# Optimization experiments

Hardware: AMD Instinct MI355X
Metric: run time of the kernel (lower is better)

The kernel has to match this reference:

```python
import jax, jax.numpy as jnp
import numpy as np

ATOM_DIM, HID, N_LAYERS, N_HEADS, PF_DIM = 34, 256, 2, 8, 1024
B, NA, NP = 32, 512, 1024


def setup_inputs() -> dict:
    key = jax.random.key(0)
    ks = iter(jax.random.split(key, 32))
    def rn(shape, s=0.02):
        return jax.random.normal(next(ks), shape, dtype=jnp.float32) * s
    L = N_LAYERS
    z = lambda *s: jnp.zeros(s, jnp.float32)
    return {
        "trg": jax.random.normal(next(ks), (B, NA, ATOM_DIM), dtype=jnp.float32),
        "src": jax.random.normal(next(ks), (B, NP, HID), dtype=jnp.float32),
        "ft_w": rn((HID, ATOM_DIM)), "ft_b": z(HID),
        "ln_g": jnp.ones((L, HID), jnp.float32), "ln_b": z(L, HID),
        "sa_wq": rn((L, HID, HID)), "sa_bq": z(L, HID),
        "sa_wk": rn((L, HID, HID)), "sa_bk": z(L, HID),
        "sa_wv": rn((L, HID, HID)), "sa_bv": z(L, HID),
        "sa_wf": rn((L, HID, HID)), "sa_bf": z(L, HID),
        "ea_wq": rn((L, HID, HID)), "ea_bq": z(L, HID),
        "ea_wk": rn((L, HID, HID)), "ea_bk": z(L, HID),
        "ea_wv": rn((L, HID, HID)), "ea_bv": z(L, HID),
        "ea_wf": rn((L, HID, HID)), "ea_bf": z(L, HID),
        "pf_w1": rn((L, PF_DIM, HID)), "pf_b1": z(L, PF_DIM),
        "pf_w2": rn((L, HID, PF_DIM)), "pf_b2": z(L, HID),
        "fc1_w": rn((256, HID)), "fc1_b": z(256),
        "fc2_w": rn((2, 256)), "fc2_b": z(2),
    }


def _ln(x, g, b, eps=1e-5):
    m = jnp.mean(x, axis=-1, keepdims=True)
    v = jnp.mean(jnp.square(x - m), axis=-1, keepdims=True)
    return (x - m) * jax.lax.rsqrt(v + eps) * g + b


def _attn(xq, xkv, wq, bq, wk, bk, wv, bv, wf, bf):
    b_, lq, h = xq.shape
    d = h // N_HEADS
    q = (xq @ wq.T + bq).reshape(b_, lq, N_HEADS, d).transpose(0, 2, 1, 3)
    k = (xkv @ wk.T + bk).reshape(b_, -1, N_HEADS, d).transpose(0, 2, 1, 3)
    v = (xkv @ wv.T + bv).reshape(b_, -1, N_HEADS, d).transpose(0, 2, 1, 3)
    scale = jnp.sqrt(jnp.float32(d))  # TransformerCPI: sqrt(hid_dim // n_heads)
    a = jax.nn.softmax(jnp.einsum('bhqd,bhkd->bhqk', q, k) / scale, axis=-1)
    o = jnp.einsum('bhqk,bhkd->bhqd', a, v).transpose(0, 2, 1, 3).reshape(b_, lq, h)
    return o @ wf.T + bf


def reference(trg, src, ft_w, ft_b, ln_g, ln_b,
              sa_wq, sa_bq, sa_wk, sa_bk, sa_wv, sa_bv, sa_wf, sa_bf,
              ea_wq, ea_bq, ea_wk, ea_bk, ea_wv, ea_bv, ea_wf, ea_bf,
              pf_w1, pf_b1, pf_w2, pf_b2, fc1_w, fc1_b, fc2_w, fc2_b):
    x = trg @ ft_w.T + ft_b  # [B, NA, HID]
    for l in range(N_LAYERS):
        x = _ln(x + _attn(x, x, sa_wq[l], sa_bq[l], sa_wk[l], sa_bk[l],
                          sa_wv[l], sa_bv[l], sa_wf[l], sa_bf[l]), ln_g[l], ln_b[l])
        x = _ln(x + _attn(x, src, ea_wq[l], ea_bq[l], ea_wk[l], ea_bk[l],
                          ea_wv[l], ea_bv[l], ea_wf[l], ea_bf[l]), ln_g[l], ln_b[l])
        h = jax.nn.relu(x @ pf_w1[l].T + pf_b1[l]) @ pf_w2[l].T + pf_b2[l]
        x = _ln(x + h, ln_g[l], ln_b[l])
    # norm-weighted attention pooling (replaces the nested Python loops)
    w = jax.nn.softmax(jnp.linalg.norm(x, axis=2), axis=1)  # [B, NA]
    pooled = jnp.einsum('bn,bnh->bh', w, x)  # [B, HID]
    return jax.nn.relu(pooled @ fc1_w.T + fc1_b) @ fc2_w.T + fc2_b
```

## Files before the change

kernel.cpp:

```cpp
#include <hip/hip_runtime.h>
#include <hip/hip_bf16.h>
#include <math.h>

#define B_   32
#define NA   512
#define NP   1024
#define HID  256
#define NH   8
#define DH   32
#define PF   1024

typedef short bf16x8 __attribute__((ext_vector_type(8)));
typedef float f32x4  __attribute__((ext_vector_type(4)));
typedef float f32x16 __attribute__((ext_vector_type(16)));

#define ZERO16 {0.f,0.f,0.f,0.f,0.f,0.f,0.f,0.f,0.f,0.f,0.f,0.f,0.f,0.f,0.f,0.f}

static __device__ inline unsigned short f2bf(float f) {
    __hip_bfloat16 h = __float2bfloat16(f);
    unsigned short u;
    __builtin_memcpy(&u, &h, 2);
    return u;
}
static __device__ inline bf16x8 pack8(float4 a, float4 b) {
    bf16x8 r;
    r[0] = (short)f2bf(a.x); r[1] = (short)f2bf(a.y);
    r[2] = (short)f2bf(a.z); r[3] = (short)f2bf(a.w);
    r[4] = (short)f2bf(b.x); r[5] = (short)f2bf(b.y);
    r[6] = (short)f2bf(b.z); r[7] = (short)f2bf(b.w);
    return r;
}

__global__ __launch_bounds__(256) void ft_kernel(const float* __restrict__ trg,
    const float* __restrict__ w, const float* __restrict__ b,
    float* __restrict__ out, unsigned short* __restrict__ outb)
{
    __shared__ float Ws[256][35];
    int tid = threadIdx.x;
    for (int k = 0; k < 34; ++k) Ws[tid][k] = w[tid*34 + k];
    float bias = b[tid];
    __syncthreads();
    int m0 = blockIdx.x * 32;
    for (int r = 0; r < 32; ++r) {
        int m = m0 + r;
        const float* tr = trg + (size_t)m*34;
        float acc = bias;
        #pragma unroll
        for (int k = 0; k < 34; ++k) acc += tr[k] * Ws[tid][k];
        out [(size_t)m*HID + tid] = acc;
        outb[(size_t)m*HID + tid] = f2bf(acc);
    }
}

__global__ __launch_bounds__(256) void cvt_bf16(const float* __restrict__ in,
    unsigned short* __restrict__ outb, int n8)
{
    int i = blockIdx.x*256 + threadIdx.x;
    int stride = gridDim.x*256;
    for (; i < n8; i += stride) {
        float4 a = *(const float4*)(in + (size_t)i*8);
        float4 b = *(const float4*)(in + (size_t)i*8 + 4);
        *(bf16x8*)(outb + (size_t)i*8) = pack8(a, b);
    }
}

__global__ __launch_bounds__(256) void cvt_w(
    const float* __restrict__ s0, const float* __restrict__ s1,
    const float* __restrict__ s2, const float* __restrict__ s3,
    const float* __restrict__ s4, const float* __restrict__ s5,
    const float* __restrict__ s6, const float* __restrict__ s7,
    const float* __restrict__ s8, const float* __restrict__ s9,
    unsigned short* __restrict__ dst)
{
    const int z = blockIdx.z;
    const float* src;
    switch (z) {
        case 0: src = s0; break; case 1: src = s1; break;
        case 2: src = s2; break; case 3: src = s3; break;
        case 4: src = s4; break; case 5: src = s5; break;
        case 6: src = s6; break; case 7: src = s7; break;
        case 8: src = s8; break; default: src = s9; break;
    }
    const int n8 = (z < 8) ? 16384 : 65536;
    const size_t off = (z < 8) ? (size_t)z*131072 : (1048576u + (size_t)(z-8)*524288);
    unsigned short* o = dst + off;
    int i = blockIdx.x*256 + threadIdx.x;
    const int stride = gridDim.x*256;
    for (; i < n8; i += stride) {
        float4 a = *(const float4*)(src + (size_t)i*8);
        float4 b = *(const float4*)(src + (size_t)i*8 + 4);
        *(bf16x8*)(o + (size_t)i*8) = pack8(a, b);
    }
}

static __device__ inline void gemm_core(const unsigned short* __restrict__ Ab,
    const unsigned short* __restrict__ Wb, const float* __restrict__ bias,
    void* __restrict__ Cv, int M, int N, int K, int mode, int L, float oscale,
    int bx, int by)
{
    __shared__ __attribute__((aligned(16))) unsigned short As[128][72];
    __shared__ __attribute__((aligned(16))) unsigned short Bs[64][72];
    const int tid = threadIdx.x;
    const int wave = tid >> 6, lane = tid & 63, lq = lane & 15, g = lane >> 4;
    const int wr = wave >> 1, wc = wave & 1;
    const int m0 = by * 128, n0 = bx * 64;

    const int ar = tid >> 1, ac = (tid & 1) * 32;
    const int br = tid >> 2, bc = (tid & 3) * 16;

    f32x4 acc[4][2] = {};
    bf16x8 sa[4], sw[2];

    auto LOAD = [&](int kt) {
        const int k0 = kt * 64;
        const unsigned short* Ap = Ab + (size_t)(m0 + ar)*K + k0 + ac;
        #pragma unroll
        for (int i = 0; i < 4; ++i)
            sa[i] = *(const bf16x8*)(Ap + i*8);
        const unsigned short* Wp = Wb + (size_t)(n0 + br)*K + k0 + bc;
        #pragma unroll
        for (int i = 0; i < 2; ++i)
            sw[i] = *(const bf16x8*)(Wp + i*8);
    };
    auto STORE = [&]() {
        #pragma unroll
        for (int i = 0; i < 4; ++i) *(bf16x8*)&As[ar][ac + i*8] = sa[i];
        #pragma unroll
        for (int i = 0; i < 2; ++i) *(bf16x8*)&Bs[br][bc + i*8] = sw[i];
    };

    const int nk = K / 64;
    LOAD(0);
    for (int kt = 0; kt < nk; ++kt) {
        __syncthreads();
        STORE();
        __syncthreads();
        if (kt + 1 < nk) LOAD(kt + 1);
        #pragma unroll
        for (int ks = 0; ks < 2; ++ks) {
            bf16x8 bf0 = *(const bf16x8*)&Bs[wc*32 +  0 + lq][ks*32 + g*8];
            bf16x8 bf1 = *(const bf16x8*)&Bs[wc*32 + 16 + lq][ks*32 + g*8];
            #pragma unroll
            for (int i = 0; i < 4; ++i) {
                bf16x8 af = *(const bf16x8*)&As[wr*64 + i*16 + lq][ks*32 + g*8];
                acc[i][0] = __builtin_amdgcn_mfma_f32_16x16x32_bf16(af, bf0, acc[i][0], 0, 0, 0);
                acc[i][1] = __builtin_amdgcn_mfma_f32_16x16x32_bf16(af, bf1, acc[i][1], 0, 0, 0);
            }
        }
    }

    float bb[2];
    #pragma unroll
    for (int j = 0; j < 2; ++j) bb[j] = bias[n0 + wc*32 + j*16 + lq];

    #pragma unroll
    for (int i = 0; i < 4; ++i) {
        const int mb = m0 + wr*64 + i*16 + 4*g;
        #pragma unroll
        for (int j = 0; j < 2; ++j) {
            const int n = n0 + wc*32 + j*16 + lq;
            f32x4 v = acc[i][j];
            #pragma unroll
            for (int r = 0; r < 4; ++r) v[r] = (v[r] + bb[j]) * oscale;
            if (mode == 0) {
                float* Cf = (float*)Cv;
                #pragma unroll
                for (int r = 0; r < 4; ++r) Cf[(size_t)(mb + r)*N + n] = v[r];
            } else if (mode == 1) {
                unsigned short* Cb = (unsigned short*)Cv;
                #pragma unroll
                for (int r = 0; r < 4; ++r) Cb[(size_t)(mb + r)*N + n] = f2bf(v[r]);
            } else if (mode == 3) {
                unsigned short* Cb = (unsigned short*)Cv;
                #pragma unroll
                for (int r = 0; r < 4; ++r) Cb[(size_t)(mb + r)*N + n] = f2bf(fmaxf(v[r], 0.f));
            } else {
                unsigned short* Cb = (unsigned short*)Cv;
                const int bI = mb / L, kk = mb % L;
                const int hh = n >> 5, d0 = n & 31;
                ushort4 pk;
                pk.x = f2bf(v[0]); pk.y = f2bf(v[1]); pk.z = f2bf(v[2]); pk.w = f2bf(v[3]);
                *(ushort4*)(Cb + ((size_t)(bI*NH + hh)*DH + d0)*L + kk) = pk;
            }
        }
    }
}

__global__ __launch_bounds__(256) void gemm_mfma(const unsigned short* __restrict__ A,
    const unsigned short* __restrict__ W, const float* __restrict__ bias,
    void* __restrict__ C, int M, int N, int K, int mode, int L)
{
    gemm_core(A, W, bias, C, M, N, K, mode, L, 1.f, blockIdx.x, blockIdx.y);
}

__global__ __launch_bounds__(256) void qkv_mfma(const unsigned short* __restrict__ Aq,
    const unsigned short* __restrict__ Akv,
    const unsigned short* __restrict__ Wq, const float* __restrict__ bq,
    const unsigned short* __restrict__ Wk, const float* __restrict__ bk,
    const unsigned short* __restrict__ Wv, const float* __restrict__ bv,
    void* __restrict__ qo, void* __restrict__ ko, void* __restrict__ vo,
    int Mq, int Mkv, int L)
{
    const int z = blockIdx.z;
    const unsigned short* A = (z == 0) ? Aq : Akv;
    const unsigned short* W = (z == 0) ? Wq : ((z == 1) ? Wk : Wv);
    const float* bb = (z == 0) ? bq : ((z == 1) ? bk : bv);
    void* C = (z == 0) ? qo : ((z == 1) ? ko : vo);
    const int M = (z == 0) ? Mq : Mkv;
    const int mode = (z == 2) ? 2 : 1;
    const float sc = (z == 0) ? 0.17677669529663687f : 1.f;
    if ((int)blockIdx.y * 128 >= M) return;
    gemm_core(A, W, bb, C, M, HID, HID, mode, L, sc, blockIdx.x, blockIdx.y);
}

__global__ __launch_bounds__(256) void attn_mfma(const unsigned short* __restrict__ Qb,
    const unsigned short* __restrict__ Kb, const unsigned short* __restrict__ VTb,
    unsigned short* __restrict__ O, int Lk)
{
    __shared__ __attribute__((aligned(16))) unsigned short Kl[64][40];
    __shared__ __attribute__((aligned(16))) unsigned short Vl[32][72];
    __shared__ __attribute__((aligned(16))) unsigned short Pl[4][32][72];
    __shared__ __attribute__((aligned(16))) float Ll[4][32];
    const int b = blockIdx.z, h = blockIdx.y, qt = blockIdx.x;
    const int tid = threadIdx.x, w = tid >> 6, lane = tid & 63;
    const int q32 = lane & 31, hi = lane >> 5;

    const unsigned short* qp = Qb + ((size_t)(b*NA + qt*128 + w*32 + q32))*HID + h*DH + hi*8;
    bf16x8 qf0 = *(const bf16x8*)qp;
    bf16x8 qf1 = *(const bf16x8*)(qp + 16);

    const unsigned short* Kg = Kb  + ((size_t)b*Lk)*HID + h*DH;
    const unsigned short* Vg = VTb + ((size_t)(b*NH + h))*DH*Lk;

    const int kr = tid >> 2, kc = (tid & 3) * 8;
    const int vr = tid >> 3, vc = (tid & 7) * 8;

    f32x16 o = ZERO16;
    float lacc = 0.f;

    bf16x8 kreg, vreg;
    auto LOADKV = [&](int kt0) {
        kreg = *(const bf16x8*)(Kg + (size_t)(kt0 + kr)*HID + kc);
        vreg = *(const bf16x8*)(Vg + (size_t)vr*Lk + kt0 + vc);
    };

    LOADKV(0);
    for (int kt0 = 0; kt0 < Lk; kt0 += 64) {
        __syncthreads();
        *(bf16x8*)&Kl[kr][kc] = kreg;
        *(bf16x8*)&Vl[vr][vc] = vreg;
        __syncthreads();
        if (kt0 + 64 < Lk) LOADKV(kt0 + 64);

        f32x16 st0 = ZERO16, st1 = ZERO16;
        {
            bf16x8 k00 = *(const bf16x8*)&Kl[q32     ][hi*8];
            bf16x8 k01 = *(const bf16x8*)&Kl[q32     ][16 + hi*8];
            bf16x8 k10 = *(const bf16x8*)&Kl[32 + q32][hi*8];
            bf16x8 k11 = *(const bf16x8*)&Kl[32 + q32][16 + hi*8];
            st0 = __builtin_amdgcn_mfma_f32_32x32x16_bf16(k00, qf0, st0, 0, 0, 0);
            st0 = __builtin_amdgcn_mfma_f32_32x32x16_bf16(k01, qf1, st0, 0, 0, 0);
            st1 = __builtin_amdgcn_mfma_f32_32x32x16_bf16(k10, qf0, st1, 0, 0, 0);
            st1 = __builtin_amdgcn_mfma_f32_32x32x16_bf16(k11, qf1, st1, 0, 0, 0);
        }
        float lp = 0.f;
        #pragma unroll
        for (int t = 0; t < 2; ++t) {
            const f32x16& stt = t ? st1 : st0;
            #pragma unroll
            for (int jg = 0; jg < 4; ++jg) {
                float p0 = __expf(stt[jg*4+0]), p1 = __expf(stt[jg*4+1]);
                float p2 = __expf(stt[jg*4+2]), p3 = __expf(stt[jg*4+3]);
                lp += p0 + p1 + p2 + p3;
                ushort4 pk;
                pk.x = f2bf(p0); pk.y = f2bf(p1); pk.z = f2bf(p2); pk.w = f2bf(p3);
                *(ushort4*)&Pl[w][q32][t*32 + jg*8 + hi*4] = pk;
            }
        }
        lacc += lp;
        #pragma unroll
        for (int c = 0; c < 4; ++c) {
            bf16x8 pf = *(const bf16x8*)&Pl[w][q32][c*16 + hi*8];
            bf16x8 vf = *(const bf16x8*)&Vl[q32][c*16 + hi*8];
            o = __builtin_amdgcn_mfma_f32_32x32x16_bf16(pf, vf, o, 0, 0, 0);
        }
    }

    float lt = lacc + __shfl_xor(lacc, 32);
    float linv = 1.f / lt;
    if (hi == 0) Ll[w][q32] = linv;
    f32x4 li[4];
    #pragma unroll
    for (int jg = 0; jg < 4; ++jg) li[jg] = *(const f32x4*)&Ll[w][jg*8 + hi*4];

    unsigned short* Op = O + ((size_t)(b*NA + qt*128 + w*32))*HID + h*DH + q32;
    #pragma unroll
    for (int jg = 0; jg < 4; ++jg) {
        #pragma unroll
        for (int r2 = 0; r2 < 4; ++r2) {
            const int q = jg*8 + hi*4 + r2;
            Op[(size_t)q*HID] = f2bf(o[jg*4 + r2] * li[jg][r2]);
            (void)0;
        }
    }
}

__global__ __launch_bounds__(256) void add_ln(float* __restrict__ x,
    const float* __restrict__ t, const float* __restrict__ g,
    const float* __restrict__ bt, unsigned short* __restrict__ xb)
{
    const int row = blockIdx.x*4 + (threadIdx.x >> 6);
    const int lane = threadIdx.x & 63;
    const size_t base = (size_t)row*HID + lane*4;
    float4 v = *(const float4*)(x + base);
    float4 tv = *(const float4*)(t + base);
    v.x += tv.x; v.y += tv.y; v.z += tv.z; v.w += tv.w;
    float s = v.x + v.y + v.z + v.w;
    #pragma unroll
    for (int o = 32; o > 0; o >>= 1) s += __shfl_xor(s, o);
    float mean = s * (1.f/256.f);
    float4 d = {v.x - mean, v.y - mean, v.z - mean, v.w - mean};
    float q2 = d.x*d.x + d.y*d.y + d.z*d.z + d.w*d.w;
    #pragma unroll
    for (int o = 32; o > 0; o >>= 1) q2 += __shfl_xor(q2, o);
    float rs = rsqrtf(q2*(1.f/256.f) + 1e-5f);
    float4 gv = *(const float4*)(g + lane*4);
    float4 bv = *(const float4*)(bt + lane*4);
    float4 ov;
    ov.x = d.x*rs*gv.x + bv.x; ov.y = d.y*rs*gv.y + bv.y;
    ov.z = d.z*rs*gv.z + bv.z; ov.w = d.w*rs*gv.w + bv.w;
    *(float4*)(x + base) = ov;
    ushort4 pk;
    pk.x = f2bf(ov.x); pk.y = f2bf(ov.y); pk.z = f2bf(ov.z); pk.w = f2bf(ov.w);
    *(ushort4*)(xb + base) = pk;
}

__global__ __launch_bounds__(256) void norms_k(const float* __restrict__ x,
    float* __restrict__ nw)
{
    const int row = blockIdx.x*4 + (threadIdx.x >> 6);
    const int lane = threadIdx.x & 63;
    float4 v = *(const float4*)(x + (size_t)row*HID + lane*4);
    float s = v.x*v.x + v.y*v.y + v.z*v.z + v.w*v.w;
    #pragma unroll
    for (int o = 32; o > 0; o >>= 1) s += __shfl_xor(s, o);
    if (lane == 0) nw[row] = sqrtf(s);
}

__global__ __launch_bounds__(256) void pooled_k(const float* __restrict__ x,
    const float* __restrict__ nw, float* __restrict__ pooled)
{
    __shared__ float sw[NA];
    __shared__ float red[256];
    __shared__ float part[8][33];
    const int b = blockIdx.x, hc = blockIdx.y;
    const int tid = threadIdx.x;
    const float* nb = nw + (size_t)b*NA;
    float v0 = nb[tid], v1 = nb[tid + 256];
    red[tid] = fmaxf(v0, v1); __syncthreads();
    for (int s = 128; s > 0; s >>= 1) { if (tid < s) red[tid] = fmaxf(red[tid], red[tid+s]); __syncthreads(); }
    float mx = red[0]; __syncthreads();
    float e0 = __expf(v0 - mx), e1 = __expf(v1 - mx);
    sw[tid] = e0; sw[tid + 256] = e1;
    red[tid] = e0 + e1; __syncthreads();
    for (int s = 128; s > 0; s >>= 1) { if (tid < s) red[tid] += red[tid+s]; __syncthreads(); }
    float inv = 1.f / red[0];
    __syncthreads();
    const int ng = tid >> 5, col = tid & 31;
    const float* xp = x + (size_t)b*NA*HID + hc*32 + col;
    float acc = 0.f;
    for (int n = ng; n < NA; n += 8)
        acc += sw[n] * xp[(size_t)n*HID];
    part[ng][col] = acc;
    __syncthreads();
    if (tid < 32) {
        float s = 0.f;
        #pragma unroll
        for (int i = 0; i < 8; ++i) s += part[i][tid];
        pooled[(size_t)b*HID + hc*32 + tid] = s * inv;
    }
}

__global__ __launch_bounds__(256) void head_k(const float* __restrict__ pooled,
    const float* __restrict__ fc1w, const float* __restrict__ fc1b,
    const float* __restrict__ fc2w, const float* __restrict__ fc2b,
    float* __restrict__ out)
{
    __shared__ float p[HID];
    __shared__ float a1[HID];
    const int b = blockIdx.x, tid = threadIdx.x;
    p[tid] = pooled[(size_t)b*HID + tid];
    __syncthreads();
    float s1 = fc1b[tid];
    const float* w1 = fc1w + (size_t)tid*HID;
    for (int k2 = 0; k2 < HID; k2 += 4) {
        float4 w = *(const float4*)(w1 + k2);
        s1 += p[k2]*w.x + p[k2+1]*w.y + p[k2+2]*w.z + p[k2+3]*w.w;
    }
    a1[tid] = fmaxf(s1, 0.f);
    __syncthreads();
    if (tid < 2) {
        float s2 = fc2b[tid];
        const float* w2 = fc2w + (size_t)tid*HID;
        for (int k2 = 0; k2 < HID; ++k2) s2 += a1[k2] * w2[k2];
        out[b*2 + tid] = s2;
    }
}

extern "C" void kernel_launch(void* const* d_in, const int* in_sizes, int n_in,
                              void* d_out, int out_size, void* d_ws, size_t ws_size,
                              hipStream_t stream)
{
    const float* trg  = (const float*)d_in[0];
    const float* src  = (const float*)d_in[1];
    const float* ft_w = (const float*)d_in[2];
    const float* ft_b = (const float*)d_in[3];
    const float* ln_g = (const float*)d_in[4];
    const float* ln_b = (const float*)d_in[5];
    const float* sa_wq = (const float*)d_in[6];  const float* sa_bq = (const float*)d_in[7];
    const float* sa_wk = (const float*)d_in[8];  const float* sa_bk = (const float*)d_in[9];
    const float* sa_wv = (const float*)d_in[10]; const float* sa_bv = (const float*)d_in[11];
    const float* sa_wf = (const float*)d_in[12]; const float* sa_bf = (const float*)d_in[13];
    const float* ea_wq = (const float*)d_in[14]; const float* ea_bq = (const float*)d_in[15];
    const float* ea_wk = (const float*)d_in[16]; const float* ea_bk = (const float*)d_in[17];
    const float* ea_wv = (const float*)d_in[18]; const float* ea_bv = (const float*)d_in[19];
    const float* ea_wf = (const float*)d_in[20]; const float* ea_bf = (const float*)d_in[21];
    const float* pf_w1 = (const float*)d_in[22]; const float* pf_b1 = (const float*)d_in[23];
    const float* pf_w2 = (const float*)d_in[24]; const float* pf_b2 = (const float*)d_in[25];
    const float* fc1w  = (const float*)d_in[26]; const float* fc1b  = (const float*)d_in[27];
    const float* fc2w  = (const float*)d_in[28]; const float* fc2b  = (const float*)d_in[29];
    float* out = (float*)d_out;

    const size_t NTOK = (size_t)B_*NA;
    const size_t NSRC = (size_t)B_*NP;
    float* ws = (float*)d_ws;
    float* x  = ws;
    float* u  = x + NTOK*HID;
    float* nw = u + NTOK*HID;
    float* pooled = nw + NTOK;
    unsigned short* xb   = (unsigned short*)(pooled + B_*HID);
    unsigned short* tb   = xb + NTOK*HID;
    unsigned short* srcb = tb + NTOK*HID;
    unsigned short* qb   = srcb + NSRC*HID;
    unsigned short* kb   = qb + NTOK*HID;
    unsigned short* vTb  = kb + NSRC*HID;
    unsigned short* wb   = vTb + NSRC*HID;
    unsigned short* hb   = qb;

    unsigned short* saq_b = wb;
    unsigned short* sak_b = wb +  131072;
    unsigned short* sav_b = wb +  262144;
    unsigned short* saf_b = wb +  393216;
    unsigned short* eaq_b = wb +  524288;
    unsigned short* eak_b = wb +  655360;
    unsigned short* eav_b = wb +  786432;
    unsigned short* eaf_b = wb +  917504;
    unsigned short* pw1_b = wb + 1048576;
    unsigned short* pw2_b = wb + 1572864;

    const int M = (int)NTOK;
    dim3 blk(256);

    cvt_w<<<dim3(64, 1, 10), blk, 0, stream>>>(sa_wq, sa_wk, sa_wv, sa_wf,
        ea_wq, ea_wk, ea_wv, ea_wf, pf_w1, pf_w2, wb);
    ft_kernel<<<M/32, blk, 0, stream>>>(trg, ft_w, ft_b, x, xb);
    cvt_bf16<<<1024, blk, 0, stream>>>(src, srcb, (int)(NSRC*HID/8));

    for (int l = 0; l < 2; ++l) {
        const size_t wo = (size_t)l*HID*HID, bo = (size_t)l*HID;
        qkv_mfma<<<dim3(HID/64, M/128, 3), blk, 0, stream>>>(xb, xb,
            saq_b+wo, sa_bq+bo, sak_b+wo, sa_bk+bo, sav_b+wo, sa_bv+bo,
            qb, kb, vTb, M, M, NA);
        attn_mfma<<<dim3(NA/128, NH, B_), blk, 0, stream>>>(qb, kb, vTb, tb, NA);
        gemm_mfma<<<dim3(HID/64, M/128), blk, 0, stream>>>(tb, saf_b+wo, sa_bf+bo, u, M, HID, HID, 0, 0);
        add_ln<<<M/4, blk, 0, stream>>>(x, u, ln_g+bo, ln_b+bo, xb);
        qkv_mfma<<<dim3(HID/64, (int)NSRC/128, 3), blk, 0, stream>>>(xb, srcb,
            eaq_b+wo, ea_bq+bo, eak_b+wo, ea_bk+bo, eav_b+wo, ea_bv+bo,
            qb, kb, vTb, M, (int)NSRC, NP);
        attn_mfma<<<dim3(NA/128, NH, B_), blk, 0, stream>>>(qb, kb, vTb, tb, NP);
        gemm_mfma<<<dim3(HID/64, M/128), blk, 0, stream>>>(tb, eaf_b+wo, ea_bf+bo, u, M, HID, HID, 0, 0);
        add_ln<<<M/4, blk, 0, stream>>>(x, u, ln_g+bo, ln_b+bo, xb);
        gemm_mfma<<<dim3(PF/64, M/128), blk, 0, stream>>>(xb, pw1_b+(size_t)l*PF*HID, pf_b1+(size_t)l*PF, hb, M, PF, HID, 3, 0);
        gemm_mfma<<<dim3(HID/64, M/128), blk, 0, stream>>>(hb, pw2_b+(size_t)l*HID*PF, pf_b2+bo, u, M, HID, PF, 0, 0);
        add_ln<<<M/4, blk, 0, stream>>>(x, u, ln_g+bo, ln_b+bo, xb);
    }

    norms_k<<<M/4, blk, 0, stream>>>(x, nw);
    pooled_k<<<dim3(B_, 8), blk, 0, stream>>>(x, nw, pooled);
    head_k<<<B_, blk, 0, stream>>>(pooled, fc1w, fc1b, fc2w, fc2b, out);
}
```

Measured before the change: 508.8 us.

## Load K/V fragments directly to registers and shuffle P via permlane in attention

The attention kernel no longer stages K, V and P tiles through shared memory with block-wide barriers. Each wave loads its MFMA K and V fragments straight from global memory into registers, double-buffered across two 64-key tiles. The P matrix is rearranged into the MFMA operand layout with permlane32_swap instead of an LDS round trip. exp is replaced by exp2, with log2(e) folded into the Q scale. This removes LDS traffic and barriers but duplicates global loads across the four waves of a block and raises register pressure.

```diff
diff --git a/kernel.cpp b/kernel.cpp
--- a/kernel.cpp
+++ b/kernel.cpp
@@ -13,6 +13,7 @@
 typedef short bf16x8 __attribute__((ext_vector_type(8)));
 typedef float f32x4  __attribute__((ext_vector_type(4)));
 typedef float f32x16 __attribute__((ext_vector_type(16)));
+typedef unsigned u32x4 __attribute__((ext_vector_type(4)));
 
 #define ZERO16 {0.f,0.f,0.f,0.f,0.f,0.f,0.f,0.f,0.f,0.f,0.f,0.f,0.f,0.f,0.f,0.f}
 
@@ -21,6 +22,9 @@
     unsigned short u;
     __builtin_memcpy(&u, &h, 2);
     return u;
+}
+static __device__ inline unsigned cvtpk(float lo, float hi) {
+    return (unsigned)f2bf(lo) | ((unsigned)f2bf(hi) << 16);
 }
 static __device__ inline bf16x8 pack8(float4 a, float4 b) {
     bf16x8 r;
@@ -208,7 +212,7 @@
     void* C = (z == 0) ? qo : ((z == 1) ? ko : vo);
     const int M = (z == 0) ? Mq : Mkv;
     const int mode = (z == 2) ? 2 : 1;
-    const float sc = (z == 0) ? 0.17677669529663687f : 1.f;
+    const float sc = (z == 0) ? 0.25504082364238727f : 1.f;
     if ((int)blockIdx.y * 128 >= M) return;
     gemm_core(A, W, bb, C, M, HID, HID, mode, L, sc, blockIdx.x, blockIdx.y);
 }
@@ -217,10 +221,7 @@
     const unsigned short* __restrict__ Kb, const unsigned short* __restrict__ VTb,
     unsigned short* __restrict__ O, int Lk)
 {
-    __shared__ __attribute__((aligned(16))) unsigned short Kl[64][40];
-    __shared__ __attribute__((aligned(16))) unsigned short Vl[32][72];
-    __shared__ __attribute__((aligned(16))) unsigned short Pl[4][32][72];
-    __shared__ __attribute__((aligned(16))) float Ll[4][32];
+    __shared__ float Ll[4][32];
     const int b = blockIdx.z, h = blockIdx.y, qt = blockIdx.x;
     const int tid = threadIdx.x, w = tid >> 6, lane = tid & 63;
     const int q32 = lane & 31, hi = lane >> 5;
@@ -229,61 +230,63 @@
     bf16x8 qf0 = *(const bf16x8*)qp;
     bf16x8 qf1 = *(const bf16x8*)(qp + 16);
 
-    const unsigned short* Kg = Kb  + ((size_t)b*Lk)*HID + h*DH;
-    const unsigned short* Vg = VTb + ((size_t)(b*NH + h))*DH*Lk;
-
-    const int kr = tid >> 2, kc = (tid & 3) * 8;
-    const int vr = tid >> 3, vc = (tid & 7) * 8;
+    const unsigned short* Kr = Kb  + ((size_t)(b*Lk + q32))*HID + h*DH + hi*8;
+    const unsigned short* Vr = VTb + ((size_t)((b*NH + h)*DH + q32))*Lk + hi*8;
 
     f32x16 o = ZERO16;
     float lacc = 0.f;
 
-    bf16x8 kreg, vreg;
-    auto LOADKV = [&](int kt0) {
-        kreg = *(const bf16x8*)(Kg + (size_t)(kt0 + kr)*HID + kc);
-        vreg = *(const bf16x8*)(Vg + (size_t)vr*Lk + kt0 + vc);
+    bf16x8 kfA[4], vfA[4], kfB[4], vfB[4];
+    auto LOADT = [&](int kt0, bf16x8* kd, bf16x8* vd) {
+        #pragma unroll
+        for (int t = 0; t < 2; ++t)
+            #pragma unroll
+            for (int dc = 0; dc < 2; ++dc)
+                kd[t*2+dc] = *(const bf16x8*)(Kr + (size_t)(kt0 + 32*t)*HID + dc*16);
+        #pragma unroll
+        for (int c = 0; c < 4; ++c)
+            vd[c] = *(const bf16x8*)(Vr + kt0 + c*16);
     };
-
-    LOADKV(0);
-    for (int kt0 = 0; kt0 < Lk; kt0 += 64) {
-        __syncthreads();
-        *(bf16x8*)&Kl[kr][kc] = kreg;
-        *(bf16x8*)&Vl[vr][vc] = vreg;
-        __syncthreads();
-        if (kt0 + 64 < Lk) LOADKV(kt0 + 64);
-
+    auto COMPUTE = [&](const bf16x8* kf, const bf16x8* vf) {
         f32x16 st0 = ZERO16, st1 = ZERO16;
-        {
-            bf16x8 k00 = *(const bf16x8*)&Kl[q32     ][hi*8];
-            bf16x8 k01 = *(const bf16x8*)&Kl[q32     ][16 + hi*8];
-            bf16x8 k10 = *(const bf16x8*)&Kl[32 + q32][hi*8];
-            bf16x8 k11 = *(const bf16x8*)&Kl[32 + q32][16 + hi*8];
-            st0 = __builtin_amdgcn_mfma_f32_32x32x16_bf16(k00, qf0, st0, 0, 0, 0);
-            st0 = __builtin_amdgcn_mfma_f32_32x32x16_bf16(k01, qf1, st0, 0, 0, 0);
-            st1 = __builtin_amdgcn_mfma_f32_32x32x16_bf16(k10, qf0, st1, 0, 0, 0);
-            st1 = __builtin_amdgcn_mfma_f32_32x32x16_bf16(k11, qf1, st1, 0, 0, 0);
-        }
+        st0 = __builtin_amdgcn_mfma_f32_32x32x16_bf16(kf[0], qf0, st0, 0, 0, 0);
+        st0 = __builtin_amdgcn_mfma_f32_32x32x16_bf16(kf[1], qf1, st0, 0, 0, 0);
+        st1 = __builtin_amdgcn_mfma_f32_32x32x16_bf16(kf[2], qf0, st1, 0, 0, 0);
+        st1 = __builtin_amdgcn_mfma_f32_32x32x16_bf16(kf[3], qf1, st1, 0, 0, 0);
+        bf16x8 pa[4];
         float lp = 0.f;
         #pragma unroll
-        for (int t = 0; t < 2; ++t) {
-            const f32x16& stt = t ? st1 : st0;
-            #pragma unroll
-            for (int jg = 0; jg < 4; ++jg) {
-                float p0 = __expf(stt[jg*4+0]), p1 = __expf(stt[jg*4+1]);
-                float p2 = __expf(stt[jg*4+2]), p3 = __expf(stt[jg*4+3]);
-                lp += p0 + p1 + p2 + p3;
-                ushort4 pk;
-                pk.x = f2bf(p0); pk.y = f2bf(p1); pk.z = f2bf(p2); pk.w = f2bf(p3);
-                *(ushort4*)&Pl[w][q32][t*32 + jg*8 + hi*4] = pk;
-            }
+        for (int c = 0; c < 4; ++c) {
+            const f32x16& s = (c < 2) ? st0 : st1;
+            const int rb = (c & 1) * 8;
+            float p0 = __builtin_amdgcn_exp2f(s[rb+0]);
+            float p1 = __builtin_amdgcn_exp2f(s[rb+1]);
+            float p2 = __builtin_amdgcn_exp2f(s[rb+2]);
+            float p3 = __builtin_amdgcn_exp2f(s[rb+3]);
+            float p4 = __builtin_amdgcn_exp2f(s[rb+4]);
+            float p5 = __builtin_amdgcn_exp2f(s[rb+5]);
+            float p6 = __builtin_amdgcn_exp2f(s[rb+6]);
+            float p7 = __builtin_amdgcn_exp2f(s[rb+7]);
+            lp += (p0+p1) + (p2+p3) + (p4+p5) + (p6+p7);
+            unsigned A1 = cvtpk(p0, p1), A2 = cvtpk(p2, p3);
+            unsigned B1 = cvtpk(p4, p5), B2 = cvtpk(p6, p7);
+            auto r1 = __builtin_amdgcn_permlane32_swap(A1, B1, false, false);
+            auto r2 = __builtin_amdgcn_permlane32_swap(A2, B2, false, false);
+            u32x4 pw; pw[0] = r1[0]; pw[1] = r2[0]; pw[2] = r1[1]; pw[3] = r2[1];
+            __builtin_memcpy(&pa[c], &pw, 16);
         }
         lacc += lp;
         #pragma unroll
-        for (int c = 0; c < 4; ++c) {
-            bf16x8 pf = *(const bf16x8*)&Pl[w][q32][c*16 + hi*8];
-            bf16x8 vf = *(const bf16x8*)&Vl[q32][c*16 + hi*8];
-            o = __builtin_amdgcn_mfma_f32_32x32x16_bf16(pf, vf, o, 0, 0, 0);
-        }
+        for (int c = 0; c < 4; ++c)
+            o = __builtin_amdgcn_mfma_f32_32x32x16_bf16(pa[c], vf[c], o, 0, 0, 0);
+    };
+
+    LOADT(0, kfA, vfA);
+    for (int kt0 = 0; kt0 < Lk; kt0 += 128) {
+        LOADT(kt0 + 64, kfB, vfB);
+        COMPUTE(kfA, vfA);
+        if (kt0 + 128 < Lk) LOADT(kt0 + 128, kfA, vfA);
+        COMPUTE(kfB, vfB);
     }
 
     float lt = lacc + __shfl_xor(lacc, 32);
@@ -300,7 +303,6 @@
         for (int r2 = 0; r2 < 4; ++r2) {
             const int q = jg*8 + hi*4 + r2;
             Op[(size_t)q*HID] = f2bf(o[jg*4 + r2] * li[jg][r2]);
-            (void)0;
         }
     }
 }
```

New measurement: 578.5 us. 1.14x slower.
